# Kernel tuning notes

Measured on AMD Instinct MI355X. Metric: run time of the kernel, lower is better.

The kernel has to match this reference:

```python
import jax, jax.numpy as jnp
import numpy as np

EMBED_DIM = 1024
NUM_HEADS = 16
HEAD_DIM = EMBED_DIM // NUM_HEADS
LN_EPS = 1e-5


def setup_inputs() -> dict:
    key = jax.random.key(0)
    ks = jax.random.split(key, 13)
    b, n_q, k_len, E = 4, 2048, 2048, EMBED_DIM
    s = 1.0 / np.sqrt(E)
    inp = {
        "Q_input": jax.random.normal(ks[0], (b, n_q, E), jnp.float32),
        "K_input": jax.random.normal(ks[1], (b, k_len, E), jnp.float32),
        "V_input": jax.random.normal(ks[2], (b, k_len, E), jnp.float32),
        "Wq": jax.random.normal(ks[3], (E, E), jnp.float32) * s,
        "bq": jnp.zeros((E,), jnp.float32),
        "Wk": jax.random.normal(ks[4], (E, E), jnp.float32) * s,
        "bk": jnp.zeros((E,), jnp.float32),
        "Wv": jax.random.normal(ks[5], (E, E), jnp.float32) * s,
        "bv": jnp.zeros((E,), jnp.float32),
        "Wo": jax.random.normal(ks[6], (E, E), jnp.float32) * s,
        "bo": jnp.zeros((E,), jnp.float32),
        "gamma": jnp.ones((E,), jnp.float32),
        "beta": jnp.zeros((E,), jnp.float32),
    }
    return inp


def _layer_norm(x, gamma, beta):
    mu = jnp.mean(x, axis=-1, keepdims=True)
    var = jnp.mean(jnp.square(x - mu), axis=-1, keepdims=True)
    return (x - mu) * jax.lax.rsqrt(var + LN_EPS) * gamma + beta


def reference(Q_input, K_input, V_input, Wq, bq, Wk, bk, Wv, bv, Wo, bo, gamma, beta):
    b, n_q, E = Q_input.shape
    k_len = K_input.shape[1]
    H, D = NUM_HEADS, HEAD_DIM
    # projections (Linear: x @ W^T + b; here W stored as [E_in, E_out])
    Q = (Q_input @ Wq + bq).reshape(b, n_q, H, D).transpose(0, 2, 1, 3)   # [b,H,n_q,D]
    K = (K_input @ Wk + bk).reshape(b, k_len, H, D).transpose(0, 2, 1, 3)  # [b,H,k,D]
    V = (V_input @ Wv + bv).reshape(b, k_len, H, D).transpose(0, 2, 1, 3)
    scores = jnp.einsum('bhqd,bhkd->bhqk', Q, K) / jnp.sqrt(jnp.float32(D))
    attn = jax.nn.softmax(scores, axis=-1)
    ctx = jnp.einsum('bhqk,bhkd->bhqd', attn, V)           # [b,H,n_q,D]
    ctx = ctx.transpose(0, 2, 1, 3).reshape(b, n_q, E)
    out = ctx @ Wo + bo                                    # dropout = identity (eval)
    return _layer_norm(Q_input + out, gamma, beta)
```

## Files before the change

kernel.cpp:

```cpp
#include <hip/hip_runtime.h>

typedef __attribute__((ext_vector_type(8))) short s8v;
typedef __attribute__((ext_vector_type(4))) short s4v;
typedef __attribute__((ext_vector_type(4))) float f4v;

#define MFMA16(a, b, c) __builtin_amdgcn_mfma_f32_16x16x32_bf16((a), (b), (c), 0, 0, 0)
#define AS1 __attribute__((address_space(1)))
#define AS3 __attribute__((address_space(3)))

__device__ __forceinline__ short f2bf(float f) {
  union { float f; unsigned u; } v; v.f = f;
  unsigned r = v.u + 0x7FFFu + ((v.u >> 16) & 1u);
  return (short)(r >> 16);
}
__device__ __forceinline__ float bf2f(short s) {
  union { unsigned u; float f; } v; v.u = ((unsigned)(unsigned short)s) << 16;
  return v.f;
}
__device__ __forceinline__ unsigned fbits(float f) {
  union { float f; unsigned u; } v; v.f = f; return v.u;
}
__device__ __forceinline__ unsigned pack2(float hi, float lo) {
  return __builtin_amdgcn_perm(fbits(hi), fbits(lo), 0x07060302u);
}
__device__ __forceinline__ unsigned pack2rn(float hi, float lo) {
  return __builtin_amdgcn_perm(fbits(hi) + 0x8000u, fbits(lo) + 0x8000u, 0x07060302u);
}
__device__ __forceinline__ void gld16(const void* g, void* l) {
  __builtin_amdgcn_global_load_lds((const AS1 unsigned*)g, (AS3 unsigned*)l, 16, 0, 0);
}

__global__ __launch_bounds__(256) void wtrans4(const float* __restrict__ W0,
                                               const float* __restrict__ W1,
                                               const float* __restrict__ W2,
                                               const float* __restrict__ W3,
                                               short* __restrict__ Wt) {
  const float* W = blockIdx.z == 0 ? W0 : blockIdx.z == 1 ? W1 : blockIdx.z == 2 ? W2 : W3;
  Wt += (size_t)blockIdx.z * 1048576;
  __shared__ float tile[64][65];
  const int r0 = blockIdx.y * 64, c0 = blockIdx.x * 64;
  const int t = threadIdx.x;
  for (int i = 0; i < 4; ++i) {
    int lin = t + i * 256;
    int row = lin >> 4, c4 = (lin & 15) << 2;
    float4 v = *(const float4*)(W + (size_t)(r0 + row) * 1024 + c0 + c4);
    tile[row][c4 + 0] = v.x; tile[row][c4 + 1] = v.y;
    tile[row][c4 + 2] = v.z; tile[row][c4 + 3] = v.w;
  }
  __syncthreads();
  for (int i = 0; i < 4; ++i) {
    int lin = t + i * 256;
    int nl = lin >> 4, k4 = (lin & 15) << 2;
    s4v sv = { f2bf(tile[k4 + 0][nl]), f2bf(tile[k4 + 1][nl]),
               f2bf(tile[k4 + 2][nl]), f2bf(tile[k4 + 3][nl]) };
    *(s4v*)&Wt[(size_t)(c0 + nl) * 1024 + r0 + k4] = sv;
  }
}

__global__ __launch_bounds__(256) void cast_a(const float* __restrict__ A0,
                                              const float* __restrict__ A1,
                                              const float* __restrict__ A2,
                                              short* __restrict__ outb) {
  const float* A = blockIdx.y == 0 ? A0 : blockIdx.y == 1 ? A1 : A2;
  short* o = outb + (size_t)blockIdx.y * 8388608;
  const size_t base = ((size_t)blockIdx.x * 256 + threadIdx.x) * 16;
  const float4 v0 = *(const float4*)(A + base);
  const float4 v1 = *(const float4*)(A + base + 4);
  const float4 v2 = *(const float4*)(A + base + 8);
  const float4 v3 = *(const float4*)(A + base + 12);
  union { s8v v; unsigned u[4]; } p0, p1;
  p0.u[0] = pack2rn(v0.y, v0.x); p0.u[1] = pack2rn(v0.w, v0.z);
  p0.u[2] = pack2rn(v1.y, v1.x); p0.u[3] = pack2rn(v1.w, v1.z);
  p1.u[0] = pack2rn(v2.y, v2.x); p1.u[1] = pack2rn(v2.w, v2.z);
  p1.u[2] = pack2rn(v3.y, v3.x); p1.u[3] = pack2rn(v3.w, v3.z);
  *(s8v*)(o + base) = p0.v;
  *(s8v*)(o + base + 8) = p1.v;
}

#define GLDA(j, bb, kt) gld16(Asrc[j] + (size_t)(kt) * 64, &smem[(bb) + ldsA + (j) * 4096])
#define GLDB(j, bb, kt) gld16(Bsrc[j] + (size_t)(kt) * 64, &smem[(bb) + 8192 + ldsA + (j) * 4096])

template <int EPI>
__global__ __launch_bounds__(512, 2) void gemm8p(
    const short* __restrict__ Ab, const short* __restrict__ Bt,
    const float* __restrict__ b0, const float* __restrict__ b1,
    const float* __restrict__ b2, float s0,
    short* __restrict__ outb) {
  __shared__ __align__(16) short smem[73728];

  const int z = blockIdx.z;
  Ab += (size_t)z * 8388608;
  Bt += (size_t)z * 1048576;
  outb += (size_t)z * 8388608;
  const float* bias = z == 0 ? b0 : z == 1 ? b1 : b2;
  const float scale = z == 0 ? s0 : 1.f;

  const int tid = threadIdx.x;
  const int lane = tid & 63, w = tid >> 6;
  const int quad = lane >> 4, l16 = lane & 15;
  const int wm = (w >> 2) * 64, wn = (w & 3) * 64;
  const int mBase = blockIdx.x * 128, nBase = blockIdx.y * 256;

  f4v acc[4][4] = {};

  const short* Asrc[2];
  const short* Bsrc[4];
#pragma unroll
  for (int j = 0; j < 2; ++j) {
    int s = tid + j * 512;
    Asrc[j] = Ab + (size_t)(mBase + (s >> 3)) * 1024 + (((s & 7) ^ ((s >> 3) & 7)) << 3);
  }
#pragma unroll
  for (int j = 0; j < 4; ++j) {
    int s = tid + j * 512;
    Bsrc[j] = Bt + (size_t)(nBase + (s >> 3)) * 1024 + (((s & 7) ^ ((s >> 3) & 7)) << 3);
  }
  const int ldsA = tid * 8;

  int axk[2];
#pragma unroll
  for (int kh = 0; kh < 2; ++kh) axk[kh] = (((kh * 4 + quad) ^ (l16 & 7)) << 3);
  const int arow = (wm + l16) * 64;
  const int brow = 8192 + (wn + l16) * 64;

#pragma unroll
  for (int t = 0; t < 3; ++t) {
    const int bb = t * 24576;
    GLDB(0, bb, t); GLDB(1, bb, t); GLDB(2, bb, t); GLDB(3, bb, t);
    GLDA(0, bb, t); GLDA(1, bb, t);
  }
  asm volatile("s_waitcnt vmcnt(12)" ::: "memory");
  __builtin_amdgcn_s_barrier();

  int cb = 0, sb = 49152;
#pragma unroll 1
  for (int kt = 0; kt < 16; ++kt) {
    const bool st = (kt + 2) < 16;
    s8v a[4][2], b[4][2];
#pragma unroll
    for (int kh = 0; kh < 2; ++kh) {
      b[0][kh] = *(const s8v*)&smem[cb + brow + 0 * 1024 + axk[kh]];
      b[1][kh] = *(const s8v*)&smem[cb + brow + 1 * 1024 + axk[kh]];
      a[0][kh] = *(const s8v*)&smem[cb + arow + 0 * 1024 + axk[kh]];
      a[1][kh] = *(const s8v*)&smem[cb + arow + 1 * 1024 + axk[kh]];
    }
    if (st) { GLDB(0, sb, kt + 2); GLDB(1, sb, kt + 2); }
    __builtin_amdgcn_s_barrier();
    __builtin_amdgcn_s_setprio(1);
#pragma unroll
    for (int nt = 0; nt < 2; ++nt)
#pragma unroll
      for (int mt = 0; mt < 2; ++mt)
#pragma unroll
        for (int kh = 0; kh < 2; ++kh)
          acc[nt][mt] = MFMA16(b[nt][kh], a[mt][kh], acc[nt][mt]);
    __builtin_amdgcn_s_setprio(0);
    __builtin_amdgcn_s_barrier();
#pragma unroll
    for (int kh = 0; kh < 2; ++kh) {
      b[2][kh] = *(const s8v*)&smem[cb + brow + 2 * 1024 + axk[kh]];
      b[3][kh] = *(const s8v*)&smem[cb + brow + 3 * 1024 + axk[kh]];
    }
    if (st) { GLDB(2, sb, kt + 2); GLDB(3, sb, kt + 2); }
    __builtin_amdgcn_s_barrier();
    __builtin_amdgcn_s_setprio(1);
#pragma unroll
    for (int nt = 2; nt < 4; ++nt)
#pragma unroll
      for (int mt = 0; mt < 2; ++mt)
#pragma unroll
        for (int kh = 0; kh < 2; ++kh)
          acc[nt][mt] = MFMA16(b[nt][kh], a[mt][kh], acc[nt][mt]);
    __builtin_amdgcn_s_setprio(0);
    __builtin_amdgcn_s_barrier();
#pragma unroll
    for (int kh = 0; kh < 2; ++kh) {
      a[2][kh] = *(const s8v*)&smem[cb + arow + 2 * 1024 + axk[kh]];
      a[3][kh] = *(const s8v*)&smem[cb + arow + 3 * 1024 + axk[kh]];
    }
    if (st) { GLDA(0, sb, kt + 2); }
    __builtin_amdgcn_s_barrier();
    __builtin_amdgcn_s_setprio(1);
#pragma unroll
    for (int nt = 2; nt < 4; ++nt)
#pragma unroll
      for (int mt = 2; mt < 4; ++mt)
#pragma unroll
        for (int kh = 0; kh < 2; ++kh)
          acc[nt][mt] = MFMA16(b[nt][kh], a[mt][kh], acc[nt][mt]);
    __builtin_amdgcn_s_setprio(0);
    __builtin_amdgcn_s_barrier();
    if (st) { GLDA(1, sb, kt + 2); }
    __builtin_amdgcn_s_barrier();
    __builtin_amdgcn_s_setprio(1);
#pragma unroll
    for (int nt = 0; nt < 2; ++nt)
#pragma unroll
      for (int mt = 2; mt < 4; ++mt)
#pragma unroll
        for (int kh = 0; kh < 2; ++kh)
          acc[nt][mt] = MFMA16(b[nt][kh], a[mt][kh], acc[nt][mt]);
    __builtin_amdgcn_s_setprio(0);
    if (kt < 14) {
      asm volatile("s_waitcnt vmcnt(6)" ::: "memory");
    } else if (kt == 14) {
      asm volatile("s_waitcnt vmcnt(0)" ::: "memory");
    }
    if (kt < 15) __builtin_amdgcn_s_barrier();
    cb = (cb == 49152) ? 0 : cb + 24576;
    sb = (sb == 49152) ? 0 : sb + 24576;
  }

  f4v bv_[4];
#pragma unroll
  for (int nt = 0; nt < 4; ++nt)
    bv_[nt] = *(const f4v*)&bias[nBase + wn + nt * 16 + quad * 4];

  const int bI = mBase >> 11, tok0 = mBase & 2047;
  const bool vpath = (EPI == 0) && (z == 2);
  if (vpath) {
    short (*Tv)[136] = (short(*)[136])smem;
#pragma unroll
    for (int nt = 0; nt < 4; ++nt)
#pragma unroll
      for (int r = 0; r < 4; ++r) {
        int feat = wn + nt * 16 + quad * 4 + r;
#pragma unroll
        for (int mt = 0; mt < 4; ++mt)
          Tv[feat][wm + mt * 16 + l16] = f2bf(acc[nt][mt][r] + bv_[nt][r]);
      }
    __syncthreads();
#pragma unroll
    for (int it = 0; it < 8; ++it) {
      int id = tid + it * 512;
      int f = id >> 4, t8 = (id & 15) << 3;
      s8v v = *(const s8v*)&Tv[f][t8];
      int gf = nBase + f, h = gf >> 6, d = gf & 63;
      *(s8v*)&outb[(((size_t)bI * 16 + h) * 64 + d) * 2048 + tok0 + t8] = v;
    }
  } else {
    short (*Ta)[264] = (short(*)[264])smem;
#pragma unroll
    for (int nt = 0; nt < 4; ++nt)
#pragma unroll
      for (int mt = 0; mt < 4; ++mt) {
        union { s4v v; unsigned u[2]; } pk;
        pk.u[0] = pack2rn((acc[nt][mt][1] + bv_[nt][1]) * scale,
                          (acc[nt][mt][0] + bv_[nt][0]) * scale);
        pk.u[1] = pack2rn((acc[nt][mt][3] + bv_[nt][3]) * scale,
                          (acc[nt][mt][2] + bv_[nt][2]) * scale);
        *(s4v*)&Ta[wm + mt * 16 + l16][wn + nt * 16 + quad * 4] = pk.v;
      }
    __syncthreads();
#pragma unroll
    for (int it = 0; it < 8; ++it) {
      int id = tid + it * 512;
      int tok = id >> 5, f8 = (id & 31) << 3;
      s8v v = *(const s8v*)&Ta[tok][f8];
      if constexpr (EPI == 1) {
        *(s8v*)&outb[(size_t)(mBase + tok) * 1024 + nBase + f8] = v;
      } else {
        int gf = nBase + f8, h = gf >> 6, d = gf & 63;
        *(s8v*)&outb[(((size_t)bI * 16 + h) * 2048 + tok0 + tok) * 64 + d] = v;
      }
    }
  }
}

__global__ __launch_bounds__(256, 2) void attn_kernel(
    const short* __restrict__ Qp, const short* __restrict__ Kp,
    const short* __restrict__ Vpt, short* __restrict__ Ctx) {
  __shared__ __align__(16) short Ks[2][64][72];
  __shared__ __align__(16) short Vt[2][64][72];

  const int tid = threadIdx.x, w = tid >> 6, lane = tid & 63;
  const int quad = lane >> 4, l16 = lane & 15;
  const int qt = blockIdx.x, bh = blockIdx.y;
  const short* Qb = Qp + (size_t)bh * 2048 * 64;
  const short* Kb = Kp + (size_t)bh * 2048 * 64;
  const short* Vb = Vpt + (size_t)bh * 64 * 2048;
  const int qbase = qt * 256 + w * 64;

  int sg[2], sc8[2], sp[2];
  const short* Ksrc[2];
  const short* Vsrc[2];
#pragma unroll
  for (int i = 0; i < 2; ++i) {
    int id = tid + i * 256;
    int g = id >> 3, c8 = (id & 7) << 3;
    int p = (g & 32) | (((g >> 2) & 1) << 4) | (((g >> 3) & 3) << 2) | (g & 3);
    sg[i] = g; sc8[i] = c8; sp[i] = p;
    Ksrc[i] = Kb + (size_t)g * 64 + c8;
    Vsrc[i] = Vb + (size_t)g * 2048 + c8;
  }

  s8v qf[4][2];
#pragma unroll
  for (int mt = 0; mt < 4; ++mt)
#pragma unroll
    for (int h = 0; h < 2; ++h)
      qf[mt][h] = *(const s8v*)(Qb + (size_t)(qbase + mt * 16 + l16) * 64 + h * 32 + quad * 8);

  {
    s8v kr[2], vr[2];
#pragma unroll
    for (int i = 0; i < 2; ++i) { kr[i] = *(const s8v*)Ksrc[i]; vr[i] = *(const s8v*)Vsrc[i]; }
#pragma unroll
    for (int i = 0; i < 2; ++i) {
      *(s8v*)&Ks[0][sp[i]][sc8[i]] = kr[i];
      *(s8v*)&Vt[0][sg[i]][sc8[i]] = vr[i];
    }
  }

  const s8v vone = {16256, 16256, 16256, 16256, 16256, 16256, 16256, 16256};
  f4v Oa[4][4] = {};
  f4v La[4] = {};

  for (int kv = 0; kv < 32; ++kv) {
    const int buf = kv & 1;
    s8v kn[2], vn[2];
    if (kv < 31) {
#pragma unroll
      for (int i = 0; i < 2; ++i) {
        kn[i] = *(const s8v*)(Ksrc[i] + (size_t)(kv + 1) * 4096);
        vn[i] = *(const s8v*)(Vsrc[i] + (size_t)(kv + 1) * 64);
      }
    }
    __syncthreads();

    s8v kf[4][2], vf[4][2];
#pragma unroll
    for (int T = 0; T < 4; ++T) {
      kf[T][0] = *(const s8v*)&Ks[buf][T * 16 + l16][quad * 8];
      kf[T][1] = *(const s8v*)&Ks[buf][T * 16 + l16][32 + quad * 8];
      vf[T][0] = *(const s8v*)&Vt[buf][T * 16 + l16][quad * 8];
      vf[T][1] = *(const s8v*)&Vt[buf][T * 16 + l16][32 + quad * 8];
    }

#pragma unroll
    for (int mt = 0; mt < 4; ++mt) {
      f4v s[4] = {};
#pragma unroll
      for (int T = 0; T < 4; ++T) {
        s[T] = MFMA16(kf[T][0], qf[mt][0], s[T]);
        s[T] = MFMA16(kf[T][1], qf[mt][1], s[T]);
      }
#pragma unroll
      for (int T = 0; T < 4; ++T)
#pragma unroll
        for (int r = 0; r < 4; ++r)
          s[T][r] = __builtin_amdgcn_exp2f(s[T][r]);
      s8v pf[2];
#pragma unroll
      for (int cp = 0; cp < 2; ++cp) {
        union { s8v v; unsigned u[4]; } pk;
        pk.u[0] = pack2(s[2 * cp][1], s[2 * cp][0]);
        pk.u[1] = pack2(s[2 * cp][3], s[2 * cp][2]);
        pk.u[2] = pack2(s[2 * cp + 1][1], s[2 * cp + 1][0]);
        pk.u[3] = pack2(s[2 * cp + 1][3], s[2 * cp + 1][2]);
        pf[cp] = pk.v;
      }
      La[mt] = MFMA16(pf[0], vone, La[mt]);
      La[mt] = MFMA16(pf[1], vone, La[mt]);
#pragma unroll
      for (int nt = 0; nt < 4; ++nt) {
        Oa[mt][nt] = MFMA16(pf[0], vf[nt][0], Oa[mt][nt]);
        Oa[mt][nt] = MFMA16(pf[1], vf[nt][1], Oa[mt][nt]);
      }
    }

    if (kv < 31) {
#pragma unroll
      for (int i = 0; i < 2; ++i) {
        *(s8v*)&Ks[buf ^ 1][sp[i]][sc8[i]] = kn[i];
        *(s8v*)&Vt[buf ^ 1][sg[i]][sc8[i]] = vn[i];
      }
    }
  }

  const int b = bh >> 4, h = bh & 15;
#pragma unroll
  for (int mt = 0; mt < 4; ++mt)
#pragma unroll
    for (int r = 0; r < 4; ++r) {
      float inv = 1.f / La[mt][r];
      int q = qbase + mt * 16 + quad * 4 + r;
#pragma unroll
      for (int nt = 0; nt < 4; ++nt) {
        int d = nt * 16 + l16;
        Ctx[((size_t)b * 2048 + q) * 1024 + h * 64 + d] = f2bf(Oa[mt][nt][r] * inv);
      }
    }
}

__global__ __launch_bounds__(256) void ln_kernel(
    const float* __restrict__ resid, const short* __restrict__ attnb,
    const float* __restrict__ gamma, const float* __restrict__ beta,
    float* __restrict__ out) {
  const int row = blockIdx.x, t = threadIdx.x;
  const float4 rv = *(const float4*)(resid + (size_t)row * 1024 + t * 4);
  const s4v av = *(const s4v*)(attnb + (size_t)row * 1024 + t * 4);
  float x0 = rv.x + bf2f(av[0]), x1 = rv.y + bf2f(av[1]);
  float x2 = rv.z + bf2f(av[2]), x3 = rv.w + bf2f(av[3]);
  float s = x0 + x1 + x2 + x3;
  float ss = x0 * x0 + x1 * x1 + x2 * x2 + x3 * x3;
  for (int off = 32; off > 0; off >>= 1) {
    s += __shfl_down(s, off, 64);
    ss += __shfl_down(ss, off, 64);
  }
  __shared__ float red[8];
  const int wid = t >> 6, lane = t & 63;
  if (lane == 0) { red[wid] = s; red[4 + wid] = ss; }
  __syncthreads();
  float S = red[0] + red[1] + red[2] + red[3];
  float SS = red[4] + red[5] + red[6] + red[7];
  float mu = S * (1.f / 1024.f);
  float var = SS * (1.f / 1024.f) - mu * mu;
  float rstd = rsqrtf(var + 1e-5f);
  const float4 g = *(const float4*)(gamma + t * 4);
  const float4 bb = *(const float4*)(beta + t * 4);
  float4 o;
  o.x = (x0 - mu) * rstd * g.x + bb.x;
  o.y = (x1 - mu) * rstd * g.y + bb.y;
  o.z = (x2 - mu) * rstd * g.z + bb.z;
  o.w = (x3 - mu) * rstd * g.w + bb.w;
  *(float4*)(out + (size_t)row * 1024 + t * 4) = o;
}

extern "C" void kernel_launch(void* const* d_in, const int* in_sizes, int n_in,
                              void* d_out, int out_size, void* d_ws, size_t ws_size,
                              hipStream_t stream) {
  const float* Qin = (const float*)d_in[0];
  const float* Kin = (const float*)d_in[1];
  const float* Vin = (const float*)d_in[2];
  const float* Wq = (const float*)d_in[3];
  const float* bq = (const float*)d_in[4];
  const float* Wk = (const float*)d_in[5];
  const float* bk = (const float*)d_in[6];
  const float* Wv = (const float*)d_in[7];
  const float* bv = (const float*)d_in[8];
  const float* Wo = (const float*)d_in[9];
  const float* bo = (const float*)d_in[10];
  const float* gamma = (const float*)d_in[11];
  const float* beta = (const float*)d_in[12];
  float* out = (float*)d_out;

  char* ws = (char*)d_ws;
  const size_t MB = 1024 * 1024;
  short* Qp    = (short*)(ws);
  short* Acast = (short*)(ws + 48 * MB);
  short* Ctx   = (short*)(ws + 48 * MB);
  short* AOutB = (short*)(ws + 64 * MB);
  short* Wt    = (short*)(ws + 96 * MB);

  wtrans4<<<dim3(16, 16, 4), 256, 0, stream>>>(Wq, Wk, Wv, Wo, Wt);
  cast_a<<<dim3(2048, 3), 256, 0, stream>>>(Qin, Kin, Vin, Acast);

  const float qscale = 0.125f * 1.44269504f;

  gemm8p<0><<<dim3(64, 4, 3), 512, 0, stream>>>(
      Acast, Wt, bq, bk, bv, qscale, Qp);

  attn_kernel<<<dim3(8, 64), 256, 0, stream>>>(Qp, Qp + 8388608, Qp + 16777216, Ctx);

  gemm8p<1><<<dim3(64, 4, 1), 512, 0, stream>>>(
      Ctx, Wt + 3 * 1048576, bo, bo, bo, 1.f, AOutB);

  ln_kernel<<<8192, 256, 0, stream>>>(Qin, AOutB, gamma, beta, out);
}
```

Measured before the change: 337.3 us.

## Merge GEMM main-loop phases and remap attention blocks for XCD locality

The projection GEMM main loop goes from four barrier-separated compute phases per k-tile to two: all B fragments and the first two A fragments load up front with every B global prefetch issued at once, and the second phase loads the remaining A fragments and both A prefetches. This removes several workgroup barriers per iteration in exchange for more live fragment registers and burstier memory issue. The attention kernel also remaps block indices so that all query tiles of a given batch-head land on the same XCD, aiming for better L2 reuse of that head's K and V. The remap assumes a grid of 8 by 64 blocks.

After: 329.1 us. 2.5% less time.

```diff
diff --git a/kernel.cpp b/kernel.cpp
--- a/kernel.cpp
+++ b/kernel.cpp
@@ -141,14 +141,16 @@
     for (int kh = 0; kh < 2; ++kh) {
       b[0][kh] = *(const s8v*)&smem[cb + brow + 0 * 1024 + axk[kh]];
       b[1][kh] = *(const s8v*)&smem[cb + brow + 1 * 1024 + axk[kh]];
+      b[2][kh] = *(const s8v*)&smem[cb + brow + 2 * 1024 + axk[kh]];
+      b[3][kh] = *(const s8v*)&smem[cb + brow + 3 * 1024 + axk[kh]];
       a[0][kh] = *(const s8v*)&smem[cb + arow + 0 * 1024 + axk[kh]];
       a[1][kh] = *(const s8v*)&smem[cb + arow + 1 * 1024 + axk[kh]];
     }
-    if (st) { GLDB(0, sb, kt + 2); GLDB(1, sb, kt + 2); }
+    if (st) { GLDB(0, sb, kt + 2); GLDB(1, sb, kt + 2); GLDB(2, sb, kt + 2); GLDB(3, sb, kt + 2); }
     __builtin_amdgcn_s_barrier();
     __builtin_amdgcn_s_setprio(1);
 #pragma unroll
-    for (int nt = 0; nt < 2; ++nt)
+    for (int nt = 0; nt < 4; ++nt)
 #pragma unroll
       for (int mt = 0; mt < 2; ++mt)
 #pragma unroll
@@ -158,43 +160,14 @@
     __builtin_amdgcn_s_barrier();
 #pragma unroll
     for (int kh = 0; kh < 2; ++kh) {
-      b[2][kh] = *(const s8v*)&smem[cb + brow + 2 * 1024 + axk[kh]];
-      b[3][kh] = *(const s8v*)&smem[cb + brow + 3 * 1024 + axk[kh]];
-    }
-    if (st) { GLDB(2, sb, kt + 2); GLDB(3, sb, kt + 2); }
+      a[2][kh] = *(const s8v*)&smem[cb + arow + 2 * 1024 + axk[kh]];
+      a[3][kh] = *(const s8v*)&smem[cb + arow + 3 * 1024 + axk[kh]];
+    }
+    if (st) { GLDA(0, sb, kt + 2); GLDA(1, sb, kt + 2); }
     __builtin_amdgcn_s_barrier();
     __builtin_amdgcn_s_setprio(1);
 #pragma unroll
-    for (int nt = 2; nt < 4; ++nt)
-#pragma unroll
-      for (int mt = 0; mt < 2; ++mt)
-#pragma unroll
-        for (int kh = 0; kh < 2; ++kh)
-          acc[nt][mt] = MFMA16(b[nt][kh], a[mt][kh], acc[nt][mt]);
-    __builtin_amdgcn_s_setprio(0);
-    __builtin_amdgcn_s_barrier();
-#pragma unroll
-    for (int kh = 0; kh < 2; ++kh) {
-      a[2][kh] = *(const s8v*)&smem[cb + arow + 2 * 1024 + axk[kh]];
-      a[3][kh] = *(const s8v*)&smem[cb + arow + 3 * 1024 + axk[kh]];
-    }
-    if (st) { GLDA(0, sb, kt + 2); }
-    __builtin_amdgcn_s_barrier();
-    __builtin_amdgcn_s_setprio(1);
-#pragma unroll
-    for (int nt = 2; nt < 4; ++nt)
-#pragma unroll
-      for (int mt = 2; mt < 4; ++mt)
-#pragma unroll
-        for (int kh = 0; kh < 2; ++kh)
-          acc[nt][mt] = MFMA16(b[nt][kh], a[mt][kh], acc[nt][mt]);
-    __builtin_amdgcn_s_setprio(0);
-    __builtin_amdgcn_s_barrier();
-    if (st) { GLDA(1, sb, kt + 2); }
-    __builtin_amdgcn_s_barrier();
-    __builtin_amdgcn_s_setprio(1);
-#pragma unroll
-    for (int nt = 0; nt < 2; ++nt)
+    for (int nt = 0; nt < 4; ++nt)
 #pragma unroll
       for (int mt = 2; mt < 4; ++mt)
 #pragma unroll
@@ -275,7 +248,9 @@
 
   const int tid = threadIdx.x, w = tid >> 6, lane = tid & 63;
   const int quad = lane >> 4, l16 = lane & 15;
-  const int qt = blockIdx.x, bh = blockIdx.y;
+  const int lin = blockIdx.x + (blockIdx.y << 3);
+  const int xcd = lin & 7, j = lin >> 3;
+  const int bh = (xcd << 3) | (j >> 3), qt = j & 7;
   const short* Qb = Qp + (size_t)bh * 2048 * 64;
   const short* Kb = Kp + (size_t)bh * 2048 * 64;
   const short* Vb = Vpt + (size_t)bh * 64 * 2048;
```
